# Kernel optimization log

Measured on AMD Instinct MI355X. Metric: run time of the kernel, lower is better.

The kernel has to match this reference:

```python
import jax, jax.numpy as jnp
import numpy as np
import math

D_MODEL = 1024
NUM_HEADS = 16
THETA = 10000.0


def _rope(x, positions, theta):
    # x: (B, H, S, d_k), positions: (S,)
    d_k = x.shape[-1]
    inv_freq = 1.0 / theta ** (2.0 * jnp.arange(d_k // 2, dtype=jnp.float32) / d_k)
    angles = positions.astype(jnp.float32)[:, None] * inv_freq  # (S, d_k//2)
    cos = jnp.cos(angles)
    sin = jnp.sin(angles)
    x1 = x[..., 0::2]
    x2 = x[..., 1::2]
    r1 = x1 * cos - x2 * sin
    r2 = x1 * sin + x2 * cos
    # interleave back: (..., d_k//2, 2) -> (..., d_k)
    return jnp.stack([r1, r2], axis=-1).reshape(x.shape)


def setup_inputs() -> dict:
    key = jax.random.key(0)
    ks = jax.random.split(key, 5)
    std = math.sqrt(2.0 / (D_MODEL + D_MODEL))
    B, S = 4, 2048
    x = jax.random.normal(ks[0], (B, S, D_MODEL), dtype=jnp.float32)
    Wq = jax.random.normal(ks[1], (D_MODEL, D_MODEL), dtype=jnp.float32) * std
    Wk = jax.random.normal(ks[2], (D_MODEL, D_MODEL), dtype=jnp.float32) * std
    Wv = jax.random.normal(ks[3], (D_MODEL, D_MODEL), dtype=jnp.float32) * std
    Wo = jax.random.normal(ks[4], (D_MODEL, D_MODEL), dtype=jnp.float32) * std
    token_positions = jnp.arange(S, dtype=jnp.int32)
    return {"x": x, "Wq": Wq, "Wk": Wk, "Wv": Wv, "Wo": Wo,
            "token_positions": token_positions}


def reference(x, Wq, Wk, Wv, Wo, token_positions):
    B, S, D = x.shape
    H = NUM_HEADS
    d_k = D // H

    def proj(W):  # y = x @ W.T, split heads -> (B, H, S, d_k)
        return (x @ W.T).reshape(B, S, H, d_k).transpose(0, 2, 1, 3)

    Q = _rope(proj(Wq), token_positions, THETA)
    K = _rope(proj(Wk), token_positions, THETA)
    V = proj(Wv)

    scores = jnp.einsum('bhqd,bhkd->bhqk', Q, K) / jnp.sqrt(jnp.float32(d_k))
    causal = jnp.tril(jnp.ones((S, S), dtype=bool))  # True = attend
    scores = jnp.where(causal, scores, jnp.float32(-jnp.inf))
    attn = jax.nn.softmax(scores, axis=-1)
    out = jnp.einsum('bhqk,bhkd->bhqd', attn, V)  # (B, H, S, d_v)
    out = out.transpose(0, 2, 1, 3).reshape(B, S, D)
    return out @ Wo.T
```

## Files before the change

### kernel.cpp

```cpp
#include <hip/hip_runtime.h>
#include <hip/hip_bf16.h>

#define GAS __attribute__((address_space(1)))
#define LAS __attribute__((address_space(3)))

typedef __attribute__((ext_vector_type(8))) short bf16x8;
typedef __attribute__((ext_vector_type(4))) float f32x4;

#define D_MODEL 1024
#define NHEADS 16
#define DK 64
#define BB 4
#define SS 2048

#define SM_SCALE 0.18033688011112042f

static __device__ __forceinline__ float b2f(unsigned short u) {
  union { unsigned int i; float f; } c; c.i = ((unsigned int)u) << 16; return c.f;
}
static __device__ __forceinline__ unsigned short f2b(float f) {
  union { float f; unsigned int i; } c; c.f = f;
  unsigned int x = c.i;
  x += 0x7fffu + ((x >> 16) & 1u);
  return (unsigned short)(x >> 16);
}
static __device__ __forceinline__ unsigned int cvtpk(float lo, float hi) {
  unsigned int r;
  asm("v_cvt_pk_bf16_f32 %0, %1, %2" : "=v"(r) : "v"(lo), "v"(hi));
  return r;
}
static __device__ __forceinline__ float fexp2(float x) {
  float r;
  asm("v_exp_f32 %0, %1" : "=v"(r) : "v"(x));
  return r;
}

__global__ __launch_bounds__(256) void prep_kernel(const float* __restrict__ x,
                                                   const float* __restrict__ Wq,
                                                   const float* __restrict__ Wk,
                                                   const float* __restrict__ Wv,
                                                   const float* __restrict__ Wo,
                                                   const int* __restrict__ pos,
                                                   unsigned short* __restrict__ xb,
                                                   unsigned short* __restrict__ Wcat,
                                                   float2* __restrict__ ctab) {
  int bid = blockIdx.x;
  if (bid < 8192) {
    int i = bid * 256 + threadIdx.x;
    float4 v = reinterpret_cast<const float4*>(x)[i];
    ushort4 o;
    o.x = f2b(v.x); o.y = f2b(v.y); o.z = f2b(v.z); o.w = f2b(v.w);
    reinterpret_cast<ushort4*>(xb)[i] = o;
  } else if (bid < 12288) {
    int i = (bid - 8192) * 256 + threadIdx.x;
    int which = i >> 18, off = i & 0x3ffff;
    const float* src = which == 0 ? Wq : which == 1 ? Wk : which == 2 ? Wv : Wo;
    float4 v = reinterpret_cast<const float4*>(src)[off];
    ushort4 o;
    o.x = f2b(v.x); o.y = f2b(v.y); o.z = f2b(v.z); o.w = f2b(v.w);
    int out = i;
    if (which < 2) {
      int rr = off >> 8, inner = off & 255;
      int h = rr >> 6, dd = rr & 63;
      int rrp = h * 64 + (dd >> 1) + ((dd & 1) << 5);
      out = (which << 18) | (rrp << 8) | inner;
    }
    reinterpret_cast<ushort4*>(Wcat)[out] = o;
  } else {
    int i = (bid - 12288) * 256 + threadIdx.x;
    int s = i >> 5, pr = i & 31;
    float p = (float)pos[s];
    float ang = p * __expf(-(float)pr * 0.2878231366242557f);
    float sn, cs;
    sincosf(ang, &sn, &cs);
    ctab[i] = make_float2(cs, sn);
  }
}

static __device__ __forceinline__ void gl_lds16(const void* g, void* l) {
  __builtin_amdgcn_global_load_lds((const GAS unsigned int*)g,
                                   (LAS unsigned int*)l, 16, 0, 0);
}

template <int EPI>
__global__ __launch_bounds__(512, 2) void gemm_bt(const unsigned short* __restrict__ A,
                                                  const unsigned short* __restrict__ Bw,
                                                  void* __restrict__ outp, int N,
                                                  const float2* __restrict__ ctab) {
  const int K = 1024;
  const int NT = 16;
  __shared__ unsigned short lds_a[128 * 64];
  __shared__ unsigned short lds_b[256 * 64];
  int t = threadIdx.x;
  int lane = t & 63;
  int w = t >> 6, wr = w >> 2, wc = w & 3;
  int la = lane & 15, lg = lane >> 4;
  int b = blockIdx.x;
  int bx = ((b & 7) << 3) | ((b >> 3) & 7);
  int by = b >> 6;
  int rowBase = bx * 128;
  int colBase = by * 256;

  int c8 = t & 7, r0 = t >> 3;
  const unsigned short* Abase = A + (size_t)rowBase * K;
  const unsigned short* Bbase = Bw + (size_t)colBase * K;
  auto stage = [&](int kt) {
    int k0 = kt * 64;
#pragma unroll
    for (int i = 0; i < 2; ++i) {
      int r = r0 + i * 64;
      gl_lds16(Abase + (size_t)r * K + k0 + ((c8 ^ (r & 7)) << 3),
               &lds_a[t * 8 + i * 4096]);
    }
#pragma unroll
    for (int i = 0; i < 4; ++i) {
      int r = r0 + i * 64;
      gl_lds16(Bbase + (size_t)r * K + k0 + ((c8 ^ (r & 7)) << 3),
               &lds_b[t * 8 + i * 4096]);
    }
  };

  f32x4 acc[4][4];
#pragma unroll
  for (int i = 0; i < 4; ++i)
#pragma unroll
    for (int j = 0; j < 4; ++j) acc[i][j] = (f32x4){0.f, 0.f, 0.f, 0.f};

  for (int kt = 0; kt < NT; ++kt) {
    __syncthreads();
    stage(kt);
    __syncthreads();
#pragma unroll
    for (int s = 0; s < 2; ++s) {
      bf16x8 af[4], bfr[4];
#pragma unroll
      for (int mi = 0; mi < 4; ++mi) {
        int row = wr * 64 + mi * 16 + la;
        af[mi] = *reinterpret_cast<const bf16x8*>(
            &lds_a[row * 64 + (((s * 4 + lg) ^ (row & 7)) << 3)]);
      }
#pragma unroll
      for (int ni = 0; ni < 4; ++ni) {
        int row = wc * 64 + ni * 16 + la;
        bfr[ni] = *reinterpret_cast<const bf16x8*>(
            &lds_b[row * 64 + (((s * 4 + lg) ^ (row & 7)) << 3)]);
      }
      __builtin_amdgcn_s_setprio(1);
#pragma unroll
      for (int mi = 0; mi < 4; ++mi)
#pragma unroll
        for (int ni = 0; ni < 4; ++ni)
          acc[mi][ni] = __builtin_amdgcn_mfma_f32_16x16x32_bf16(af[mi], bfr[ni],
                                                                acc[mi][ni], 0, 0, 0);
      __builtin_amdgcn_s_setprio(0);
    }
  }

  if (EPI == 0) {
    float* out = (float*)outp;
#pragma unroll
    for (int mi = 0; mi < 4; ++mi)
#pragma unroll
      for (int ni = 0; ni < 4; ++ni)
#pragma unroll
        for (int j = 0; j < 4; ++j) {
          int row = rowBase + wr * 64 + mi * 16 + lg * 4 + j;
          int col = colBase + wc * 64 + ni * 16 + la;
          out[(size_t)row * N + col] = acc[mi][ni][j];
        }
  } else {
    unsigned short* qkv = (unsigned short*)outp;
    int col0 = colBase + wc * 64;
    int which = col0 >> 10;
    int h = (col0 & 1023) >> 6;
    if (which == 2) {
#pragma unroll
      for (int mi = 0; mi < 4; ++mi)
#pragma unroll
        for (int ni = 0; ni < 4; ++ni)
#pragma unroll
          for (int j = 0; j < 4; ++j) {
            int row = rowBase + wr * 64 + mi * 16 + lg * 4 + j;
            int dd = ni * 16 + la;
            int bb = row >> 11, s = row & 2047;
            size_t off = (size_t)2 * 8388608 +
                         ((size_t)(bb * NHEADS + h) * DK + dd) * SS + s;
            qkv[off] = f2b(acc[mi][ni][j]);
          }
    } else {
      float sc = (which == 0) ? SM_SCALE : 1.0f;
#pragma unroll
      for (int mi = 0; mi < 4; ++mi)
#pragma unroll
        for (int ni = 0; ni < 2; ++ni)
#pragma unroll
          for (int j = 0; j < 4; ++j) {
            int row = rowBase + wr * 64 + mi * 16 + lg * 4 + j;
            int bb = row >> 11, s = row & 2047;
            int pr = ni * 16 + la;
            float x1 = acc[mi][ni][j];
            float x2 = acc[mi][ni + 2][j];
            float2 cs2 = ctab[s * 32 + pr];
            float r1 = (x1 * cs2.x - x2 * cs2.y) * sc;
            float r2 = (x1 * cs2.y + x2 * cs2.x) * sc;
            size_t off = (size_t)which * 8388608 +
                         ((size_t)(bb * NHEADS + h) * SS + s) * DK + 2 * pr;
            *reinterpret_cast<unsigned int*>(&qkv[off]) = cvtpk(r1, r2);
          }
    }
  }
}

template <bool DIAG>
static __device__ __forceinline__ void smpv_tile(
    const f32x4* __restrict__ st, const unsigned short* __restrict__ vt,
    unsigned short* __restrict__ pl, int la, int lg, int kq,
    float& l, f32x4* o) {
  float rs0 = 0.f, rs1 = 0.f;
  unsigned int pk[8];
#pragma unroll
  for (int nb = 0; nb < 4; ++nb) {
#pragma unroll
    for (int jp = 0; jp < 2; ++jp) {
      float v0 = st[nb][2 * jp];
      float v1 = st[nb][2 * jp + 1];
      if (DIAG) {
        if ((nb * 16 + 2 * jp) > kq) v0 = -1e30f;
        if ((nb * 16 + 2 * jp + 1) > kq) v1 = -1e30f;
      }
      float p0 = fexp2(v0);
      float p1 = fexp2(v1);
      rs0 += p0; rs1 += p1;
      pk[nb * 2 + jp] = cvtpk(p0, p1);
    }
  }
  l += rs0 + rs1;
  char* pw = (char*)pl + la * 128;
  int sw = (la & 7) << 4;
#pragma unroll
  for (int nb = 0; nb < 4; ++nb) {
    uint2 wv; wv.x = pk[nb * 2]; wv.y = pk[nb * 2 + 1];
    *reinterpret_cast<uint2*>(pw + (((nb * 32 + lg * 8) ^ sw))) = wv;
  }
  __builtin_amdgcn_s_setprio(1);
#pragma unroll
  for (int kk = 0; kk < 2; ++kk) {
    bf16x8 pa = *reinterpret_cast<const bf16x8*>(pw + ((kk * 64 + lg * 16) ^ sw));
#pragma unroll
    for (int db = 0; db < 4; ++db) {
      int vrow = db * 16 + la;
      bf16x8 vb = *reinterpret_cast<const bf16x8*>(
          &vt[vrow * 64 + (((kk * 4 + lg) ^ (vrow & 7)) << 3)]);
      o[db] = __builtin_amdgcn_mfma_f32_16x16x32_bf16(pa, vb, o[db], 0, 0, 0);
    }
  }
  __builtin_amdgcn_s_setprio(0);
}

__global__ __launch_bounds__(256, 4) void attn_kernel(const unsigned short* __restrict__ Qh,
                                                      const unsigned short* __restrict__ Kh,
                                                      const unsigned short* __restrict__ Vt,
                                                      unsigned short* __restrict__ outA) {
  __shared__ unsigned short kbuf[2][4096];
  __shared__ unsigned short vbuf[2][4096];
  __shared__ unsigned short plds[4][1024];
  int orig = blockIdx.x;
  int xcd = orig & 7, ix = orig >> 3;
  int bh = xcd * 8 + (ix >> 4);
  int p = ix & 15;
  int qtA = p, qtB = 31 - p;
  int t = threadIdx.x, lane = t & 63, w = t >> 6;
  int la = lane & 15, lg = lane >> 4;
  int kq = w * 16 + la - lg * 4;
  const unsigned short* Qp = Qh + (size_t)bh * SS * DK;
  const unsigned short* Kp = Kh + (size_t)bh * SS * DK;
  const unsigned short* Vtp = Vt + (size_t)bh * DK * SS;
  unsigned short* plw = plds[w];

  int qrA = qtA * 64 + w * 16;
  int qrB = qtB * 64 + w * 16;
  bf16x8 qA0 = *reinterpret_cast<const bf16x8*>(Qp + (size_t)(qrA + la) * 64 + lg * 8);
  bf16x8 qA1 = *reinterpret_cast<const bf16x8*>(Qp + (size_t)(qrA + la) * 64 + 32 + lg * 8);
  bf16x8 qB0 = *reinterpret_cast<const bf16x8*>(Qp + (size_t)(qrB + la) * 64 + lg * 8);
  bf16x8 qB1 = *reinterpret_cast<const bf16x8*>(Qp + (size_t)(qrB + la) * 64 + 32 + lg * 8);

  f32x4 oA[4], oB[4];
#pragma unroll
  for (int i = 0; i < 4; ++i) {
    oA[i] = (f32x4){0.f, 0.f, 0.f, 0.f};
    oB[i] = (f32x4){0.f, 0.f, 0.f, 0.f};
  }
  float lA = 0.f, lB = 0.f;

  int c8 = t & 7, r0 = t >> 3;
  auto stage = [&](int bi, int kv) {
    int kvBase = kv * 64;
#pragma unroll
    for (int i = 0; i < 2; ++i) {
      int r = r0 + i * 32;
      gl_lds16(Kp + (size_t)(kvBase + r) * 64 + ((c8 ^ (r & 7)) << 3),
               &kbuf[bi][t * 8 + i * 2048]);
      gl_lds16(Vtp + (size_t)r * SS + kvBase + ((c8 ^ (r & 7)) << 3),
               &vbuf[bi][t * 8 + i * 2048]);
    }
  };

  stage(0, 0);
  __syncthreads();
  int cur = 0;
  for (int kv = 0; kv <= qtB; ++kv) {
    if (kv < qtB) stage(cur ^ 1, kv + 1);
    bool doA = (kv <= qtA);
    f32x4 stB[4], stA[4];
    __builtin_amdgcn_s_setprio(1);
#pragma unroll
    for (int nb = 0; nb < 4; ++nb) {
      int krow = nb * 16 + la;
      bf16x8 k0 = *reinterpret_cast<const bf16x8*>(
          &kbuf[cur][krow * 64 + ((lg ^ (krow & 7)) << 3)]);
      bf16x8 k1 = *reinterpret_cast<const bf16x8*>(
          &kbuf[cur][krow * 64 + (((4 + lg) ^ (krow & 7)) << 3)]);
      f32x4 s = (f32x4){0.f, 0.f, 0.f, 0.f};
      s = __builtin_amdgcn_mfma_f32_16x16x32_bf16(k0, qB0, s, 0, 0, 0);
      s = __builtin_amdgcn_mfma_f32_16x16x32_bf16(k1, qB1, s, 0, 0, 0);
      stB[nb] = s;
      if (doA) {
        f32x4 s2 = (f32x4){0.f, 0.f, 0.f, 0.f};
        s2 = __builtin_amdgcn_mfma_f32_16x16x32_bf16(k0, qA0, s2, 0, 0, 0);
        s2 = __builtin_amdgcn_mfma_f32_16x16x32_bf16(k1, qA1, s2, 0, 0, 0);
        stA[nb] = s2;
      }
    }
    __builtin_amdgcn_s_setprio(0);
    if (kv == qtB) smpv_tile<true>(stB, vbuf[cur], plw, la, lg, kq, lB, oB);
    else           smpv_tile<false>(stB, vbuf[cur], plw, la, lg, kq, lB, oB);
    if (doA) {
      if (kv == qtA) smpv_tile<true>(stA, vbuf[cur], plw, la, lg, kq, lA, oA);
      else           smpv_tile<false>(stA, vbuf[cur], plw, la, lg, kq, lA, oA);
    }
    __syncthreads();
    cur ^= 1;
  }

  lB += __shfl_xor(lB, 16); lB += __shfl_xor(lB, 32);
  lA += __shfl_xor(lA, 16); lA += __shfl_xor(lA, 32);

  int b = bh >> 4, h = bh & 15;
#pragma unroll
  for (int j = 0; j < 4; ++j) {
    float ljB = __shfl(lB, lg * 4 + j);
    float ljA = __shfl(lA, lg * 4 + j);
    float riB = 1.0f / ljB, riA = 1.0f / ljA;
    int qB_ = qrB + lg * 4 + j;
    int qA_ = qrA + lg * 4 + j;
#pragma unroll
    for (int db = 0; db < 4; ++db) {
      outA[((size_t)(b * SS + qB_)) * D_MODEL + h * DK + db * 16 + la] = f2b(oB[db][j] * riB);
      outA[((size_t)(b * SS + qA_)) * D_MODEL + h * DK + db * 16 + la] = f2b(oA[db][j] * riA);
    }
  }
}

extern "C" void kernel_launch(void* const* d_in, const int* in_sizes, int n_in,
                              void* d_out, int out_size, void* d_ws, size_t ws_size,
                              hipStream_t stream) {
  (void)in_sizes; (void)n_in; (void)out_size; (void)ws_size;
  const float* x  = (const float*)d_in[0];
  const float* Wq = (const float*)d_in[1];
  const float* Wk = (const float*)d_in[2];
  const float* Wv = (const float*)d_in[3];
  const float* Wo = (const float*)d_in[4];
  const int* pos  = (const int*)d_in[5];

  char* ws = (char*)d_ws;
  unsigned short* xb    = (unsigned short*)(ws);
  unsigned short* Wcat  = (unsigned short*)(ws + 16777216);
  unsigned short* Qh    = (unsigned short*)(ws + 25165824);
  unsigned short* attnO = (unsigned short*)(ws + 75497472);
  float2* ctab          = (float2*)(ws + 92274688);

  prep_kernel<<<12544, 256, 0, stream>>>(x, Wq, Wk, Wv, Wo, pos, xb, Wcat, ctab);
  gemm_bt<1><<<768, 512, 0, stream>>>(xb, Wcat, Qh, 3072, ctab);
  attn_kernel<<<1024, 256, 0, stream>>>(Qh, Qh + 8388608, Qh + 16777216, attnO);
  gemm_bt<0><<<256, 512, 0, stream>>>(attnO, Wcat + 3145728, (float*)d_out, 1024, ctab);
}
```

Before: 154.0 us.

## Double-buffer GEMM LDS tiles with K-step 32 to overlap loads and MFMA

The bt GEMM now uses two LDS buffers holding K-slices of 32 instead of one buffer holding a K-slice of 64. While the current buffer feeds the MFMAs, the next slice is prefetched into the other buffer with global_load_lds, so each iteration needs one barrier instead of two. The XOR swizzle becomes a rotation swizzle to fit the narrower 32-element rows. In exchange there are twice as many iterations and barriers, and less MFMA work between syncs to hide each load.

```diff
diff --git a/kernel.cpp b/kernel.cpp
--- a/kernel.cpp
+++ b/kernel.cpp
@@ -88,9 +88,9 @@
                                                   void* __restrict__ outp, int N,
                                                   const float2* __restrict__ ctab) {
   const int K = 1024;
-  const int NT = 16;
-  __shared__ unsigned short lds_a[128 * 64];
-  __shared__ unsigned short lds_b[256 * 64];
+  const int NT = 32;
+  __shared__ unsigned short lds_a[2][128 * 32];
+  __shared__ unsigned short lds_b[2][256 * 32];
   int t = threadIdx.x;
   int lane = t & 63;
   int w = t >> 6, wr = w >> 2, wc = w & 3;
@@ -101,22 +101,21 @@
   int rowBase = bx * 128;
   int colBase = by * 256;
 
-  int c8 = t & 7, r0 = t >> 3;
+  int cc = t & 3, r0 = t >> 2;
   const unsigned short* Abase = A + (size_t)rowBase * K;
   const unsigned short* Bbase = Bw + (size_t)colBase * K;
-  auto stage = [&](int kt) {
-    int k0 = kt * 64;
+  auto stage = [&](int bi, int kt) {
+    int k0 = kt * 32;
+    {
+      int r = r0;
+      int cg = (cc - (r >> 1)) & 3;
+      gl_lds16(Abase + (size_t)r * K + k0 + cg * 8, &lds_a[bi][t * 8]);
+    }
 #pragma unroll
     for (int i = 0; i < 2; ++i) {
-      int r = r0 + i * 64;
-      gl_lds16(Abase + (size_t)r * K + k0 + ((c8 ^ (r & 7)) << 3),
-               &lds_a[t * 8 + i * 4096]);
-    }
-#pragma unroll
-    for (int i = 0; i < 4; ++i) {
-      int r = r0 + i * 64;
-      gl_lds16(Bbase + (size_t)r * K + k0 + ((c8 ^ (r & 7)) << 3),
-               &lds_b[t * 8 + i * 4096]);
+      int r = r0 + i * 128;
+      int cg = (cc - (r >> 1)) & 3;
+      gl_lds16(Bbase + (size_t)r * K + k0 + cg * 8, &lds_b[bi][t * 8 + i * 4096]);
     }
   };
 
@@ -126,34 +125,33 @@
 #pragma unroll
     for (int j = 0; j < 4; ++j) acc[i][j] = (f32x4){0.f, 0.f, 0.f, 0.f};
 
+  stage(0, 0);
+  int cur = 0;
   for (int kt = 0; kt < NT; ++kt) {
     __syncthreads();
-    stage(kt);
-    __syncthreads();
-#pragma unroll
-    for (int s = 0; s < 2; ++s) {
-      bf16x8 af[4], bfr[4];
-#pragma unroll
-      for (int mi = 0; mi < 4; ++mi) {
-        int row = wr * 64 + mi * 16 + la;
-        af[mi] = *reinterpret_cast<const bf16x8*>(
-            &lds_a[row * 64 + (((s * 4 + lg) ^ (row & 7)) << 3)]);
-      }
-#pragma unroll
-      for (int ni = 0; ni < 4; ++ni) {
-        int row = wc * 64 + ni * 16 + la;
-        bfr[ni] = *reinterpret_cast<const bf16x8*>(
-            &lds_b[row * 64 + (((s * 4 + lg) ^ (row & 7)) << 3)]);
-      }
-      __builtin_amdgcn_s_setprio(1);
-#pragma unroll
-      for (int mi = 0; mi < 4; ++mi)
-#pragma unroll
-        for (int ni = 0; ni < 4; ++ni)
-          acc[mi][ni] = __builtin_amdgcn_mfma_f32_16x16x32_bf16(af[mi], bfr[ni],
-                                                                acc[mi][ni], 0, 0, 0);
-      __builtin_amdgcn_s_setprio(0);
-    }
+    if (kt + 1 < NT) stage(cur ^ 1, kt + 1);
+    bf16x8 af[4], bfr[4];
+#pragma unroll
+    for (int mi = 0; mi < 4; ++mi) {
+      int row = wr * 64 + mi * 16 + la;
+      af[mi] = *reinterpret_cast<const bf16x8*>(
+          &lds_a[cur][row * 32 + (((lg + (row >> 1)) & 3) << 3)]);
+    }
+#pragma unroll
+    for (int ni = 0; ni < 4; ++ni) {
+      int row = wc * 64 + ni * 16 + la;
+      bfr[ni] = *reinterpret_cast<const bf16x8*>(
+          &lds_b[cur][row * 32 + (((lg + (row >> 1)) & 3) << 3)]);
+    }
+    __builtin_amdgcn_s_setprio(1);
+#pragma unroll
+    for (int mi = 0; mi < 4; ++mi)
+#pragma unroll
+      for (int ni = 0; ni < 4; ++ni)
+        acc[mi][ni] = __builtin_amdgcn_mfma_f32_16x16x32_bf16(af[mi], bfr[ni],
+                                                              acc[mi][ni], 0, 0, 0);
+    __builtin_amdgcn_s_setprio(0);
+    cur ^= 1;
   }
 
   if (EPI == 0) {
```

Result: slower. 165.0 us (+7.1%).
